# Kernel tuning notes

Hardware: AMD Instinct MI355X
Metric: run time of the kernel (lower is better)

Reference implementation:

```python
import jax, jax.numpy as jnp
import numpy as np

EMBED_DIM = 128
HIDDEN = 64
LN_EPS = 1e-5
NORM_EPS = 1e-6


def setup_inputs() -> dict:
    key = jax.random.key(0)
    ks = jax.random.split(key, 12)
    B, L = 32, 2048
    inp = {
        "map_lane_positions": jax.random.normal(ks[0], (B, L, 10, 2), dtype=jnp.float32),
        "map_is_intersection": jax.random.randint(ks[1], (B, L), 0, 3, dtype=jnp.int64),
        "map_turn_direction": jax.random.randint(ks[2], (B, L), 0, 3, dtype=jnp.int64),
        "map_traffic_control": jax.random.randint(ks[3], (B, L), 0, 2, dtype=jnp.int64),
        # SingleInputEmbedding params: Linear(2,64) -> LayerNorm(64) -> ReLU -> Linear(64,128)
        "W1": jax.random.normal(ks[4], (2, HIDDEN), dtype=jnp.float32) * 0.5,
        "b1": jax.random.normal(ks[5], (HIDDEN,), dtype=jnp.float32) * 0.1,
        "ln_gamma": jnp.ones((HIDDEN,), dtype=jnp.float32),
        "ln_beta": jnp.zeros((HIDDEN,), dtype=jnp.float32),
        "W2": jax.random.normal(ks[6], (HIDDEN, EMBED_DIM), dtype=jnp.float32) * 0.1,
        "b2": jax.random.normal(ks[7], (EMBED_DIM,), dtype=jnp.float32) * 0.1,
        # discrete embedding tables
        "E_intersection": jax.random.normal(ks[8], (3, EMBED_DIM), dtype=jnp.float32),
        "E_turn": jax.random.normal(ks[9], (3, EMBED_DIM), dtype=jnp.float32),
        "E_traffic": jax.random.normal(ks[10], (2, EMBED_DIM), dtype=jnp.float32),
    }
    return inp


def _mlp(x, W1, b1, g, beta, W2, b2):
    h = x @ W1 + b1                                  # [..., 64]
    mu = jnp.mean(h, axis=-1, keepdims=True)
    var = jnp.mean((h - mu) ** 2, axis=-1, keepdims=True)
    h = (h - mu) * jax.lax.rsqrt(var + LN_EPS) * g + beta
    h = jax.nn.relu(h)
    return h @ W2 + b2                               # [..., 128]


def reference(map_lane_positions, map_is_intersection, map_turn_direction,
              map_traffic_control, W1, b1, ln_gamma, ln_beta, W2, b2,
              E_intersection, E_turn, E_traffic):
    # direction vectors between consecutive points: [B, L, 9, 2]
    dv = map_lane_positions[:, :, 1:, :] - map_lane_positions[:, :, :-1, :]
    norms = jnp.sqrt(jnp.sum(dv ** 2, axis=-1, keepdims=True) + NORM_EPS)
    dv = dv / norms

    cont = _mlp(dv, W1, b1, ln_gamma, ln_beta, W2, b2)   # [B, L, 9, 128]
    # discrete embeddings broadcast over the 9-point axis
    disc = (E_intersection[map_is_intersection]
            + E_turn[map_turn_direction]
            + E_traffic[map_traffic_control])             # [B, L, 128]
    fused = cont + disc[:, :, None, :]                    # [B, L, 9, 128]
    return jnp.max(fused, axis=2)                         # [B, L, 128]
```

## Files before the change

kernel.cpp:

```cpp
#include <hip/hip_runtime.h>
#include <hip/hip_bf16.h>

#define NB      16
#define THREADS 256

#define WS_CST4   0
#define WS_QUAD   256
#define WS_DISC   272
#define WS_W2     2576

typedef float f32x4  __attribute__((ext_vector_type(4)));
typedef short bf16x8 __attribute__((ext_vector_type(8)));

static __device__ __forceinline__ unsigned f2bf(float f) {
    __hip_bfloat16 h = __float2bfloat16(f);
    return (unsigned)__builtin_bit_cast(unsigned short, h);
}

__global__ __launch_bounds__(THREADS)
void lane_setup_kernel(const float* __restrict__ W1, const float* __restrict__ b1,
                       const float* __restrict__ gam, const float* __restrict__ bet,
                       const float* __restrict__ W2, const float* __restrict__ b2,
                       const float* __restrict__ Ei, const float* __restrict__ Et,
                       const float* __restrict__ Etc, float* __restrict__ ws)
{
    const int tid = threadIdx.x, lane = tid & 63, wv = tid >> 6;

    if (wv == 0) {
        float wx = W1[lane], wy = W1[64 + lane], bb = b1[lane];
        float sx = wx, sy = wy, sb = bb;
        #pragma unroll
        for (int m = 1; m < 64; m <<= 1) {
            sx += __shfl_xor(sx, m, 64);
            sy += __shfl_xor(sy, m, 64);
            sb += __shfl_xor(sb, m, 64);
        }
        float a = wx - sx * (1.f / 64.f);
        float b = wy - sy * (1.f / 64.f);
        float c = bb - sb * (1.f / 64.f);
        float p0 = a * a, p1 = b * b, p2 = a * b, p3 = a * c, p4 = b * c, p5 = c * c;
        #pragma unroll
        for (int m = 1; m < 64; m <<= 1) {
            p0 += __shfl_xor(p0, m, 64); p1 += __shfl_xor(p1, m, 64);
            p2 += __shfl_xor(p2, m, 64); p3 += __shfl_xor(p3, m, 64);
            p4 += __shfl_xor(p4, m, 64); p5 += __shfl_xor(p5, m, 64);
        }
        float g = gam[lane];
        ((float4*)(ws + WS_CST4))[lane] = make_float4(a * g, b * g, c * g, bet[lane]);
        if (lane == 0) {
            ws[WS_QUAD + 0] = p0 * (1.f / 64.f);
            ws[WS_QUAD + 1] = p1 * (1.f / 64.f);
            ws[WS_QUAD + 2] = p2 * (1.f / 64.f);
            ws[WS_QUAD + 3] = p3 * (1.f / 64.f);
            ws[WS_QUAD + 4] = p4 * (1.f / 64.f);
            ws[WS_QUAD + 5] = p5 * (1.f / 64.f) + 1e-5f;
        }
    }

    {
        uint4* dst = (uint4*)(ws + WS_W2);
        #pragma unroll
        for (int f = wv * 4; f < wv * 4 + 4; ++f) {
            int c = f >> 1, kt = f & 1;
            int col = c * 16 + (lane & 15);
            int k0  = kt * 32 + (lane >> 4) * 8;
            unsigned w[4];
            #pragma unroll
            for (int j = 0; j < 4; ++j) {
                unsigned lo = f2bf(W2[(k0 + 2 * j) * 128 + col]);
                unsigned hi = f2bf(W2[(k0 + 2 * j + 1) * 128 + col]);
                w[j] = (hi << 16) | lo;
            }
            dst[f * 64 + lane] = make_uint4(w[0], w[1], w[2], w[3]);
        }
    }

    for (int i = tid; i < 18 * 128; i += THREADS) {
        int combo = i >> 7, col = i & 127;
        int ai = combo / 6; int r = combo - ai * 6; int bi = r >> 1; int ci = r & 1;
        ws[WS_DISC + i] = b2[col] + Ei[ai * 128 + col] + Et[bi * 128 + col] + Etc[ci * 128 + col];
    }
}

__global__ __launch_bounds__(THREADS)
void lane_node_embed_mfma(const float* __restrict__ pos,
                          const int*   __restrict__ idx_int,
                          const int*   __restrict__ idx_turn,
                          const int*   __restrict__ idx_tc,
                          const float* __restrict__ ws,
                          float* __restrict__ out,
                          int n_nodes)
{
    __shared__ __align__(16) unsigned short H[NB * 9 * 64];
    __shared__ float4 smv[NB * 9];
    __shared__ int    cmb_lds[NB];

    const int tid  = threadIdx.x;
    const int lane = tid & 63;
    const int wv   = __builtin_amdgcn_readfirstlane(tid >> 6);
    const int blockStart = blockIdx.x * NB;

    if (tid < NB * 9) {
        int nd = tid / 9, p = tid - nd * 9;
        int gn = blockStart + nd;
        float ax = 0.f, ay = 0.f, is = 0.f;
        if (gn < n_nodes) {
            const float2* pp = (const float2*)pos + (size_t)gn * 10 + p;
            float2 q0 = pp[0], q1 = pp[1];
            float dx = q1.x - q0.x, dy = q1.y - q0.y;
            float inv = rsqrtf(fmaf(dx, dx, fmaf(dy, dy, 1e-6f)));
            dx *= inv; dy *= inv;
            float qA = ws[WS_QUAD + 0], qB = ws[WS_QUAD + 1], qC = ws[WS_QUAD + 2];
            float qD = ws[WS_QUAD + 3], qE = ws[WS_QUAD + 4], qF = ws[WS_QUAD + 5];
            float t   = fmaf(dx * dy, qC, fmaf(dx, qD, dy * qE));
            float var = fmaf(2.f, t, fmaf(dx * dx, qA, fmaf(dy * dy, qB, qF)));
            is = rsqrtf(var);
            ax = dx * is; ay = dy * is;
        }
        smv[tid] = make_float4(ax, ay, is, 0.f);
    }
    if (tid < NB) {
        int gn = blockStart + tid;
        cmb_lds[tid] = (gn < n_nodes)
            ? (idx_int[gn] * 3 + idx_turn[gn]) * 2 + idx_tc[gn] : 0;
    }

    const int kl   = lane & 31;
    const int half = lane >> 5;
    const float4 cstA = ((const float4*)(ws + WS_CST4))[2 * kl];
    const float4 cstB = ((const float4*)(ws + WS_CST4))[2 * kl + 1];

    const int ct0 = wv * 2;
    const uint4* wfr = (const uint4*)(ws + WS_W2);
    bf16x8 Bfr[2][2];
    #pragma unroll
    for (int c = 0; c < 2; ++c)
        #pragma unroll
        for (int kt = 0; kt < 2; ++kt)
            Bfr[c][kt] = __builtin_bit_cast(bf16x8, wfr[((ct0 + c) * 2 + kt) * 64 + lane]);

    __syncthreads();

    {
        const int kch  = kl >> 2;
        const int kofs = (2 * kl) & 7;
        #pragma unroll
        for (int i = 0; i < 2; ++i) {
            int nd = wv * 4 + 2 * i + half;
            int basew = nd * 576 + ((kch ^ (nd & 7)) << 3) + kofs;
            #pragma unroll
            for (int p = 0; p < 9; ++p) {
                float4 t = smv[nd * 9 + p];
                float a = fmaf(t.x, cstA.x, fmaf(t.y, cstA.y, fmaf(t.z, cstA.z, cstA.w)));
                float b = fmaf(t.x, cstB.x, fmaf(t.y, cstB.y, fmaf(t.z, cstB.z, cstB.w)));
                a = fmaxf(a, 0.f); b = fmaxf(b, 0.f);
                *(unsigned*)&H[basew + p * 64] = (f2bf(b) << 16) | f2bf(a);
            }
        }
    }
    __syncthreads();

    const int g   = lane >> 4;
    const int l15 = lane & 15;
    const int sr  = l15 & 7;
    const int i0  = l15 * 576 + ((g ^ sr) << 3);
    const int i1  = l15 * 576 + (((4 + g) ^ sr) << 3);

    int cjv[4];
    #pragma unroll
    for (int jj = 0; jj < 4; ++jj) cjv[jj] = cmb_lds[g * 4 + jj];
    float dvp[2][4];
    #pragma unroll
    for (int c = 0; c < 2; ++c)
        #pragma unroll
        for (int jj = 0; jj < 4; ++jj)
            dvp[c][jj] = ws[WS_DISC + cjv[jj] * 128 + (ct0 + c) * 16 + l15];

    f32x4 mx0 = {-INFINITY, -INFINITY, -INFINITY, -INFINITY};
    f32x4 mx1 = mx0;
    const f32x4 zz = {0.f, 0.f, 0.f, 0.f};
    #pragma unroll
    for (int p = 0; p < 9; ++p) {
        bf16x8 a0 = *(const bf16x8*)&H[i0 + p * 64];
        bf16x8 a1 = *(const bf16x8*)&H[i1 + p * 64];
        f32x4 t0 = __builtin_amdgcn_mfma_f32_16x16x32_bf16(a0, Bfr[0][0], zz, 0, 0, 0);
        t0       = __builtin_amdgcn_mfma_f32_16x16x32_bf16(a1, Bfr[0][1], t0, 0, 0, 0);
        f32x4 t1 = __builtin_amdgcn_mfma_f32_16x16x32_bf16(a0, Bfr[1][0], zz, 0, 0, 0);
        t1       = __builtin_amdgcn_mfma_f32_16x16x32_bf16(a1, Bfr[1][1], t1, 0, 0, 0);
        #pragma unroll
        for (int k = 0; k < 4; ++k) {
            mx0[k] = fmaxf(mx0[k], t0[k]);
            mx1[k] = fmaxf(mx1[k], t1[k]);
        }
    }

    #pragma unroll
    for (int c = 0; c < 2; ++c) {
        int col = (ct0 + c) * 16 + l15;
        f32x4 m = (c == 0) ? mx0 : mx1;
        #pragma unroll
        for (int j = 0; j < 4; ++j) {
            int gn = blockStart + g * 4 + j;
            if (gn < n_nodes)
                out[(size_t)gn * 128 + col] = m[j] + dvp[c][j];
        }
    }
}

extern "C" void kernel_launch(void* const* d_in, const int* in_sizes, int n_in,
                              void* d_out, int out_size, void* d_ws, size_t ws_size,
                              hipStream_t stream) {
    const float* pos  = (const float*)d_in[0];
    const int*   ii   = (const int*)  d_in[1];
    const int*   it   = (const int*)  d_in[2];
    const int*   itc  = (const int*)  d_in[3];
    const float* W1   = (const float*)d_in[4];
    const float* b1   = (const float*)d_in[5];
    const float* gam  = (const float*)d_in[6];
    const float* bet  = (const float*)d_in[7];
    const float* W2   = (const float*)d_in[8];
    const float* b2   = (const float*)d_in[9];
    const float* Ei   = (const float*)d_in[10];
    const float* Et   = (const float*)d_in[11];
    const float* Etc  = (const float*)d_in[12];
    float* out = (float*)d_out;
    float* ws  = (float*)d_ws;

    int n_nodes = in_sizes[1];
    int blocks  = (n_nodes + NB - 1) / NB;

    hipLaunchKernelGGL(lane_setup_kernel, dim3(1), dim3(THREADS), 0, stream,
                       W1, b1, gam, bet, W2, b2, Ei, Et, Etc, ws);
    hipLaunchKernelGGL(lane_node_embed_mfma, dim3(blocks), dim3(THREADS), 0, stream,
                       pos, ii, it, itc, ws, out, n_nodes);
}
```

Baseline: 30.45 us.

## Swap MFMA operands for float4 stores, use wave shuffles instead of LDS staging

The main kernel swaps the A/B operands of the MFMA so each lane holds four consecutive output columns of one node. The output store becomes a single float4 write per column tile, and the discrete-embedding gather becomes one float4 load per tile. The LDS staging of per-point direction vectors and combo indices, plus one __syncthreads, is replaced by per-wave computation and __shfl broadcasts, with the LN inverse-std recomputed by sqrt from the scaled vector. The setup kernel is split across 6 blocks so its three parts run in parallel, at the cost of an extra sqrt per point and duplicated index loads.

```diff
diff --git a/kernel.cpp b/kernel.cpp
--- a/kernel.cpp
+++ b/kernel.cpp
@@ -25,8 +25,9 @@
                        const float* __restrict__ Etc, float* __restrict__ ws)
 {
     const int tid = threadIdx.x, lane = tid & 63, wv = tid >> 6;
-
-    if (wv == 0) {
+    const int b = blockIdx.x;
+
+    if (b == 0 && wv == 0) {
         float wx = W1[lane], wy = W1[64 + lane], bb = b1[lane];
         float sx = wx, sy = wy, sb = bb;
         #pragma unroll
@@ -36,9 +37,9 @@
             sb += __shfl_xor(sb, m, 64);
         }
         float a = wx - sx * (1.f / 64.f);
-        float b = wy - sy * (1.f / 64.f);
+        float bc = wy - sy * (1.f / 64.f);
         float c = bb - sb * (1.f / 64.f);
-        float p0 = a * a, p1 = b * b, p2 = a * b, p3 = a * c, p4 = b * c, p5 = c * c;
+        float p0 = a * a, p1 = bc * bc, p2 = a * bc, p3 = a * c, p4 = bc * c, p5 = c * c;
         #pragma unroll
         for (int m = 1; m < 64; m <<= 1) {
             p0 += __shfl_xor(p0, m, 64); p1 += __shfl_xor(p1, m, 64);
@@ -46,7 +47,7 @@
             p4 += __shfl_xor(p4, m, 64); p5 += __shfl_xor(p5, m, 64);
         }
         float g = gam[lane];
-        ((float4*)(ws + WS_CST4))[lane] = make_float4(a * g, b * g, c * g, bet[lane]);
+        ((float4*)(ws + WS_CST4))[lane] = make_float4(a * g, bc * g, c * g, bet[lane]);
         if (lane == 0) {
             ws[WS_QUAD + 0] = p0 * (1.f / 64.f);
             ws[WS_QUAD + 1] = p1 * (1.f / 64.f);
@@ -55,30 +56,26 @@
             ws[WS_QUAD + 4] = p4 * (1.f / 64.f);
             ws[WS_QUAD + 5] = p5 * (1.f / 64.f) + 1e-5f;
         }
-    }
-
-    {
+    } else if (b >= 1 && b <= 4) {
         uint4* dst = (uint4*)(ws + WS_W2);
-        #pragma unroll
-        for (int f = wv * 4; f < wv * 4 + 4; ++f) {
-            int c = f >> 1, kt = f & 1;
-            int col = c * 16 + (lane & 15);
-            int k0  = kt * 32 + (lane >> 4) * 8;
-            unsigned w[4];
-            #pragma unroll
-            for (int j = 0; j < 4; ++j) {
-                unsigned lo = f2bf(W2[(k0 + 2 * j) * 128 + col]);
-                unsigned hi = f2bf(W2[(k0 + 2 * j + 1) * 128 + col]);
-                w[j] = (hi << 16) | lo;
-            }
-            dst[f * 64 + lane] = make_uint4(w[0], w[1], w[2], w[3]);
-        }
-    }
-
-    for (int i = tid; i < 18 * 128; i += THREADS) {
-        int combo = i >> 7, col = i & 127;
-        int ai = combo / 6; int r = combo - ai * 6; int bi = r >> 1; int ci = r & 1;
-        ws[WS_DISC + i] = b2[col] + Ei[ai * 128 + col] + Et[bi * 128 + col] + Etc[ci * 128 + col];
+        int f = (b - 1) * 4 + wv;
+        int c = f >> 1, kt = f & 1;
+        int col = c * 16 + (lane & 15);
+        int k0  = kt * 32 + (lane >> 4) * 8;
+        unsigned w[4];
+        #pragma unroll
+        for (int j = 0; j < 4; ++j) {
+            unsigned lo = f2bf(W2[(k0 + 2 * j) * 128 + col]);
+            unsigned hi = f2bf(W2[(k0 + 2 * j + 1) * 128 + col]);
+            w[j] = (hi << 16) | lo;
+        }
+        dst[f * 64 + lane] = make_uint4(w[0], w[1], w[2], w[3]);
+    } else if (b == 5) {
+        for (int i = tid; i < 18 * 128; i += THREADS) {
+            int combo = i >> 7, col = i & 127;
+            int ai = combo / 6; int r = combo - ai * 6; int bi = r >> 1; int ci = r & 1;
+            ws[WS_DISC + i] = b2[col] + Ei[ai * 128 + col] + Et[bi * 128 + col] + Etc[ci * 128 + col];
+        }
     }
 }
 
@@ -92,20 +89,22 @@
                           int n_nodes)
 {
     __shared__ __align__(16) unsigned short H[NB * 9 * 64];
-    __shared__ float4 smv[NB * 9];
-    __shared__ int    cmb_lds[NB];
 
     const int tid  = threadIdx.x;
     const int lane = tid & 63;
     const int wv   = __builtin_amdgcn_readfirstlane(tid >> 6);
     const int blockStart = blockIdx.x * NB;
 
-    if (tid < NB * 9) {
-        int nd = tid / 9, p = tid - nd * 9;
-        int gn = blockStart + nd;
-        float ax = 0.f, ay = 0.f, is = 0.f;
-        if (gn < n_nodes) {
-            const float2* pp = (const float2*)pos + (size_t)gn * 10 + p;
+    const int l15 = lane & 15;
+    const int g   = lane >> 4;
+
+    const int sn = lane / 9;
+    const int sp = lane - sn * 9;
+    float ax_own = 0.f, ay_own = 0.f;
+    {
+        int gn = blockStart + wv * 4 + sn;
+        if (lane < 36 && gn < n_nodes) {
+            const float2* pp = (const float2*)pos + (size_t)gn * 10 + sp;
             float2 q0 = pp[0], q1 = pp[1];
             float dx = q1.x - q0.x, dy = q1.y - q0.y;
             float inv = rsqrtf(fmaf(dx, dx, fmaf(dy, dy, 1e-6f)));
@@ -114,16 +113,15 @@
             float qD = ws[WS_QUAD + 3], qE = ws[WS_QUAD + 4], qF = ws[WS_QUAD + 5];
             float t   = fmaf(dx * dy, qC, fmaf(dx, qD, dy * qE));
             float var = fmaf(2.f, t, fmaf(dx * dx, qA, fmaf(dy * dy, qB, qF)));
-            is = rsqrtf(var);
-            ax = dx * is; ay = dy * is;
-        }
-        smv[tid] = make_float4(ax, ay, is, 0.f);
-    }
-    if (tid < NB) {
-        int gn = blockStart + tid;
-        cmb_lds[tid] = (gn < n_nodes)
-            ? (idx_int[gn] * 3 + idx_turn[gn]) * 2 + idx_tc[gn] : 0;
-    }
+            float is0 = rsqrtf(var);
+            ax_own = dx * is0; ay_own = dy * is0;
+        }
+    }
+
+    const int gn15 = blockStart + l15;
+    int cmb = 0;
+    if (gn15 < n_nodes)
+        cmb = (idx_int[gn15] * 3 + idx_turn[gn15]) * 2 + idx_tc[gn15];
 
     const int kl   = lane & 31;
     const int half = lane >> 5;
@@ -132,27 +130,34 @@
 
     const int ct0 = wv * 2;
     const uint4* wfr = (const uint4*)(ws + WS_W2);
-    bf16x8 Bfr[2][2];
+    bf16x8 Wfr[2][2];
     #pragma unroll
     for (int c = 0; c < 2; ++c)
         #pragma unroll
         for (int kt = 0; kt < 2; ++kt)
-            Bfr[c][kt] = __builtin_bit_cast(bf16x8, wfr[((ct0 + c) * 2 + kt) * 64 + lane]);
-
-    __syncthreads();
+            Wfr[c][kt] = __builtin_bit_cast(bf16x8, wfr[((ct0 + c) * 2 + kt) * 64 + lane]);
+
+    float4 dvp[2];
+    #pragma unroll
+    for (int c = 0; c < 2; ++c)
+        dvp[c] = *(const float4*)&ws[WS_DISC + cmb * 128 + (ct0 + c) * 16 + 4 * g];
 
     {
         const int kch  = kl >> 2;
         const int kofs = (2 * kl) & 7;
         #pragma unroll
         for (int i = 0; i < 2; ++i) {
-            int nd = wv * 4 + 2 * i + half;
+            int ndl = 2 * i + half;
+            int nd  = wv * 4 + ndl;
             int basew = nd * 576 + ((kch ^ (nd & 7)) << 3) + kofs;
             #pragma unroll
             for (int p = 0; p < 9; ++p) {
-                float4 t = smv[nd * 9 + p];
-                float a = fmaf(t.x, cstA.x, fmaf(t.y, cstA.y, fmaf(t.z, cstA.z, cstA.w)));
-                float b = fmaf(t.x, cstB.x, fmaf(t.y, cstB.y, fmaf(t.z, cstB.z, cstB.w)));
+                int o = ndl * 9 + p;
+                float ax = __shfl(ax_own, o, 64);
+                float ay = __shfl(ay_own, o, 64);
+                float is = sqrtf(fmaf(ax, ax, ay * ay));
+                float a = fmaf(ax, cstA.x, fmaf(ay, cstA.y, fmaf(is, cstA.z, cstA.w)));
+                float b = fmaf(ax, cstB.x, fmaf(ay, cstB.y, fmaf(is, cstB.z, cstB.w)));
                 a = fmaxf(a, 0.f); b = fmaxf(b, 0.f);
                 *(unsigned*)&H[basew + p * 64] = (f2bf(b) << 16) | f2bf(a);
             }
@@ -160,33 +165,21 @@
     }
     __syncthreads();
 
-    const int g   = lane >> 4;
-    const int l15 = lane & 15;
     const int sr  = l15 & 7;
     const int i0  = l15 * 576 + ((g ^ sr) << 3);
     const int i1  = l15 * 576 + (((4 + g) ^ sr) << 3);
-
-    int cjv[4];
-    #pragma unroll
-    for (int jj = 0; jj < 4; ++jj) cjv[jj] = cmb_lds[g * 4 + jj];
-    float dvp[2][4];
-    #pragma unroll
-    for (int c = 0; c < 2; ++c)
-        #pragma unroll
-        for (int jj = 0; jj < 4; ++jj)
-            dvp[c][jj] = ws[WS_DISC + cjv[jj] * 128 + (ct0 + c) * 16 + l15];
 
     f32x4 mx0 = {-INFINITY, -INFINITY, -INFINITY, -INFINITY};
     f32x4 mx1 = mx0;
     const f32x4 zz = {0.f, 0.f, 0.f, 0.f};
     #pragma unroll
     for (int p = 0; p < 9; ++p) {
-        bf16x8 a0 = *(const bf16x8*)&H[i0 + p * 64];
-        bf16x8 a1 = *(const bf16x8*)&H[i1 + p * 64];
-        f32x4 t0 = __builtin_amdgcn_mfma_f32_16x16x32_bf16(a0, Bfr[0][0], zz, 0, 0, 0);
-        t0       = __builtin_amdgcn_mfma_f32_16x16x32_bf16(a1, Bfr[0][1], t0, 0, 0, 0);
-        f32x4 t1 = __builtin_amdgcn_mfma_f32_16x16x32_bf16(a0, Bfr[1][0], zz, 0, 0, 0);
-        t1       = __builtin_amdgcn_mfma_f32_16x16x32_bf16(a1, Bfr[1][1], t1, 0, 0, 0);
+        bf16x8 h0 = *(const bf16x8*)&H[i0 + p * 64];
+        bf16x8 h1 = *(const bf16x8*)&H[i1 + p * 64];
+        f32x4 t0 = __builtin_amdgcn_mfma_f32_16x16x32_bf16(Wfr[0][0], h0, zz, 0, 0, 0);
+        t0       = __builtin_amdgcn_mfma_f32_16x16x32_bf16(Wfr[0][1], h1, t0, 0, 0, 0);
+        f32x4 t1 = __builtin_amdgcn_mfma_f32_16x16x32_bf16(Wfr[1][0], h0, zz, 0, 0, 0);
+        t1       = __builtin_amdgcn_mfma_f32_16x16x32_bf16(Wfr[1][1], h1, t1, 0, 0, 0);
         #pragma unroll
         for (int k = 0; k < 4; ++k) {
             mx0[k] = fmaxf(mx0[k], t0[k]);
@@ -194,15 +187,13 @@
         }
     }
 
-    #pragma unroll
-    for (int c = 0; c < 2; ++c) {
-        int col = (ct0 + c) * 16 + l15;
-        f32x4 m = (c == 0) ? mx0 : mx1;
-        #pragma unroll
-        for (int j = 0; j < 4; ++j) {
-            int gn = blockStart + g * 4 + j;
-            if (gn < n_nodes)
-                out[(size_t)gn * 128 + col] = m[j] + dvp[c][j];
+    if (gn15 < n_nodes) {
+        #pragma unroll
+        for (int c = 0; c < 2; ++c) {
+            f32x4 m = (c == 0) ? mx0 : mx1;
+            float4 v = make_float4(m[0] + dvp[c].x, m[1] + dvp[c].y,
+                                   m[2] + dvp[c].z, m[3] + dvp[c].w);
+            *(float4*)&out[(size_t)gn15 * 128 + (ct0 + c) * 16 + 4 * g] = v;
         }
     }
 }
@@ -229,7 +220,7 @@
     int n_nodes = in_sizes[1];
     int blocks  = (n_nodes + NB - 1) / NB;
 
-    hipLaunchKernelGGL(lane_setup_kernel, dim3(1), dim3(THREADS), 0, stream,
+    hipLaunchKernelGGL(lane_setup_kernel, dim3(6), dim3(THREADS), 0, stream,
                        W1, b1, gam, bet, W2, b2, Ei, Et, Etc, ws);
     hipLaunchKernelGGL(lane_node_embed_mfma, dim3(blocks), dim3(THREADS), 0, stream,
                        pos, ii, it, itc, ws, out, n_nodes);
```

New measurement: 38.88 us. +27.7%, slower.

## Compute direction vectors per lane in registers and split setup across blocks

Applied to the files above, without the earlier changes.

The main kernel no longer runs a separate phase that computes normalized direction vectors and LayerNorm scale into shared memory behind a barrier. Each lane now loads its node's ten points as float4 vectors and recomputes the direction, normalization and inverse std itself, which removes one __syncthreads and the smv LDS traffic at the cost of redundant math across the 32 lanes sharing a node. The setup kernel is also spread over six blocks so the W2 packing and discrete-table summation run in parallel rather than serially in one block.

```diff
diff --git a/kernel.cpp b/kernel.cpp
--- a/kernel.cpp
+++ b/kernel.cpp
@@ -25,8 +25,9 @@
                        const float* __restrict__ Etc, float* __restrict__ ws)
 {
     const int tid = threadIdx.x, lane = tid & 63, wv = tid >> 6;
-
-    if (wv == 0) {
+    const int b = blockIdx.x;
+
+    if (b == 0 && wv == 0) {
         float wx = W1[lane], wy = W1[64 + lane], bb = b1[lane];
         float sx = wx, sy = wy, sb = bb;
         #pragma unroll
@@ -36,9 +37,9 @@
             sb += __shfl_xor(sb, m, 64);
         }
         float a = wx - sx * (1.f / 64.f);
-        float b = wy - sy * (1.f / 64.f);
+        float bc = wy - sy * (1.f / 64.f);
         float c = bb - sb * (1.f / 64.f);
-        float p0 = a * a, p1 = b * b, p2 = a * b, p3 = a * c, p4 = b * c, p5 = c * c;
+        float p0 = a * a, p1 = bc * bc, p2 = a * bc, p3 = a * c, p4 = bc * c, p5 = c * c;
         #pragma unroll
         for (int m = 1; m < 64; m <<= 1) {
             p0 += __shfl_xor(p0, m, 64); p1 += __shfl_xor(p1, m, 64);
@@ -46,7 +47,7 @@
             p4 += __shfl_xor(p4, m, 64); p5 += __shfl_xor(p5, m, 64);
         }
         float g = gam[lane];
-        ((float4*)(ws + WS_CST4))[lane] = make_float4(a * g, b * g, c * g, bet[lane]);
+        ((float4*)(ws + WS_CST4))[lane] = make_float4(a * g, bc * g, c * g, bet[lane]);
         if (lane == 0) {
             ws[WS_QUAD + 0] = p0 * (1.f / 64.f);
             ws[WS_QUAD + 1] = p1 * (1.f / 64.f);
@@ -55,30 +56,26 @@
             ws[WS_QUAD + 4] = p4 * (1.f / 64.f);
             ws[WS_QUAD + 5] = p5 * (1.f / 64.f) + 1e-5f;
         }
-    }
-
-    {
+    } else if (b >= 1 && b <= 4) {
         uint4* dst = (uint4*)(ws + WS_W2);
-        #pragma unroll
-        for (int f = wv * 4; f < wv * 4 + 4; ++f) {
-            int c = f >> 1, kt = f & 1;
-            int col = c * 16 + (lane & 15);
-            int k0  = kt * 32 + (lane >> 4) * 8;
-            unsigned w[4];
-            #pragma unroll
-            for (int j = 0; j < 4; ++j) {
-                unsigned lo = f2bf(W2[(k0 + 2 * j) * 128 + col]);
-                unsigned hi = f2bf(W2[(k0 + 2 * j + 1) * 128 + col]);
-                w[j] = (hi << 16) | lo;
-            }
-            dst[f * 64 + lane] = make_uint4(w[0], w[1], w[2], w[3]);
-        }
-    }
-
-    for (int i = tid; i < 18 * 128; i += THREADS) {
-        int combo = i >> 7, col = i & 127;
-        int ai = combo / 6; int r = combo - ai * 6; int bi = r >> 1; int ci = r & 1;
-        ws[WS_DISC + i] = b2[col] + Ei[ai * 128 + col] + Et[bi * 128 + col] + Etc[ci * 128 + col];
+        int f = (b - 1) * 4 + wv;
+        int c = f >> 1, kt = f & 1;
+        int col = c * 16 + (lane & 15);
+        int k0  = kt * 32 + (lane >> 4) * 8;
+        unsigned w[4];
+        #pragma unroll
+        for (int j = 0; j < 4; ++j) {
+            unsigned lo = f2bf(W2[(k0 + 2 * j) * 128 + col]);
+            unsigned hi = f2bf(W2[(k0 + 2 * j + 1) * 128 + col]);
+            w[j] = (hi << 16) | lo;
+        }
+        dst[f * 64 + lane] = make_uint4(w[0], w[1], w[2], w[3]);
+    } else if (b == 5) {
+        for (int i = tid; i < 18 * 128; i += THREADS) {
+            int combo = i >> 7, col = i & 127;
+            int ai = combo / 6; int r = combo - ai * 6; int bi = r >> 1; int ci = r & 1;
+            ws[WS_DISC + i] = b2[col] + Ei[ai * 128 + col] + Et[bi * 128 + col] + Etc[ci * 128 + col];
+        }
     }
 }
 
@@ -92,39 +89,22 @@
                           int n_nodes)
 {
     __shared__ __align__(16) unsigned short H[NB * 9 * 64];
-    __shared__ float4 smv[NB * 9];
-    __shared__ int    cmb_lds[NB];
+    __shared__ int cmb_lds[NB];
 
     const int tid  = threadIdx.x;
     const int lane = tid & 63;
     const int wv   = __builtin_amdgcn_readfirstlane(tid >> 6);
     const int blockStart = blockIdx.x * NB;
 
-    if (tid < NB * 9) {
-        int nd = tid / 9, p = tid - nd * 9;
-        int gn = blockStart + nd;
-        float ax = 0.f, ay = 0.f, is = 0.f;
-        if (gn < n_nodes) {
-            const float2* pp = (const float2*)pos + (size_t)gn * 10 + p;
-            float2 q0 = pp[0], q1 = pp[1];
-            float dx = q1.x - q0.x, dy = q1.y - q0.y;
-            float inv = rsqrtf(fmaf(dx, dx, fmaf(dy, dy, 1e-6f)));
-            dx *= inv; dy *= inv;
-            float qA = ws[WS_QUAD + 0], qB = ws[WS_QUAD + 1], qC = ws[WS_QUAD + 2];
-            float qD = ws[WS_QUAD + 3], qE = ws[WS_QUAD + 4], qF = ws[WS_QUAD + 5];
-            float t   = fmaf(dx * dy, qC, fmaf(dx, qD, dy * qE));
-            float var = fmaf(2.f, t, fmaf(dx * dx, qA, fmaf(dy * dy, qB, qF)));
-            is = rsqrtf(var);
-            ax = dx * is; ay = dy * is;
-        }
-        smv[tid] = make_float4(ax, ay, is, 0.f);
-    }
     if (tid < NB) {
         int gn = blockStart + tid;
         cmb_lds[tid] = (gn < n_nodes)
             ? (idx_int[gn] * 3 + idx_turn[gn]) * 2 + idx_tc[gn] : 0;
     }
 
+    const float qA = ws[WS_QUAD + 0], qB = ws[WS_QUAD + 1], qC = ws[WS_QUAD + 2];
+    const float qD = ws[WS_QUAD + 3], qE = ws[WS_QUAD + 4], qF = ws[WS_QUAD + 5];
+
     const int kl   = lane & 31;
     const int half = lane >> 5;
     const float4 cstA = ((const float4*)(ws + WS_CST4))[2 * kl];
@@ -139,20 +119,42 @@
         for (int kt = 0; kt < 2; ++kt)
             Bfr[c][kt] = __builtin_bit_cast(bf16x8, wfr[((ct0 + c) * 2 + kt) * 64 + lane]);
 
-    __syncthreads();
-
     {
         const int kch  = kl >> 2;
         const int kofs = (2 * kl) & 7;
         #pragma unroll
         for (int i = 0; i < 2; ++i) {
             int nd = wv * 4 + 2 * i + half;
+            int gn = blockStart + nd;
             int basew = nd * 576 + ((kch ^ (nd & 7)) << 3) + kofs;
+
+            float4 P[5];
+            if (gn < n_nodes) {
+                const float4* pb = (const float4*)(pos + (size_t)gn * 20);
+                #pragma unroll
+                for (int j = 0; j < 5; ++j) P[j] = pb[j];
+            } else {
+                #pragma unroll
+                for (int j = 0; j < 5; ++j) P[j] = make_float4(0.f, 0.f, 0.f, 0.f);
+            }
+
             #pragma unroll
             for (int p = 0; p < 9; ++p) {
-                float4 t = smv[nd * 9 + p];
-                float a = fmaf(t.x, cstA.x, fmaf(t.y, cstA.y, fmaf(t.z, cstA.z, cstA.w)));
-                float b = fmaf(t.x, cstB.x, fmaf(t.y, cstB.y, fmaf(t.z, cstB.z, cstB.w)));
+                float x0, y0, x1, y1;
+                if ((p & 1) == 0) { x0 = P[p >> 1].x; y0 = P[p >> 1].y;
+                                    x1 = P[p >> 1].z; y1 = P[p >> 1].w; }
+                else              { x0 = P[p >> 1].z; y0 = P[p >> 1].w;
+                                    x1 = P[(p + 1) >> 1].x; y1 = P[(p + 1) >> 1].y; }
+                float dx = x1 - x0, dy = y1 - y0;
+                float inv = rsqrtf(fmaf(dx, dx, fmaf(dy, dy, 1e-6f)));
+                dx *= inv; dy *= inv;
+                float tt  = fmaf(dx * dy, qC, fmaf(dx, qD, dy * qE));
+                float var = fmaf(2.f, tt, fmaf(dx * dx, qA, fmaf(dy * dy, qB, qF)));
+                float is  = rsqrtf(var);
+                float ax = dx * is, ay = dy * is;
+
+                float a = fmaf(ax, cstA.x, fmaf(ay, cstA.y, fmaf(is, cstA.z, cstA.w)));
+                float b = fmaf(ax, cstB.x, fmaf(ay, cstB.y, fmaf(is, cstB.z, cstB.w)));
                 a = fmaxf(a, 0.f); b = fmaxf(b, 0.f);
                 *(unsigned*)&H[basew + p * 64] = (f2bf(b) << 16) | f2bf(a);
             }
@@ -229,7 +231,7 @@
     int n_nodes = in_sizes[1];
     int blocks  = (n_nodes + NB - 1) / NB;
 
-    hipLaunchKernelGGL(lane_setup_kernel, dim3(1), dim3(THREADS), 0, stream,
+    hipLaunchKernelGGL(lane_setup_kernel, dim3(6), dim3(THREADS), 0, stream,
                        W1, b1, gam, bet, W2, b2, Ei, Et, Etc, ws);
     hipLaunchKernelGGL(lane_node_embed_mfma, dim3(blocks), dim3(THREADS), 0, stream,
                        pos, ii, it, itc, ws, out, n_nodes);
```

New measurement: 39.83 us. +30.8%, slower.

## Halve nodes per block and split setup kernel across six blocks

Applied to the files above, without the earlier changes.

The main kernel now processes 8 nodes per 128-thread block instead of 16 per 256. Each wave computes four column tiles in two passes, and half of each MFMA's 16 rows are duplicates whose results are discarded. The setup kernel is split across 6 blocks so the LayerNorm constants, the W2 bf16 fragment packing and the discrete-embedding table are built in parallel rather than serially by one block. This trades wasted MFMA work for twice as many blocks, which should give better occupancy and load balance across CUs, plus a shorter setup kernel.

```diff
diff --git a/kernel.cpp b/kernel.cpp
--- a/kernel.cpp
+++ b/kernel.cpp
@@ -1,8 +1,8 @@
 #include <hip/hip_runtime.h>
 #include <hip/hip_bf16.h>
 
-#define NB      16
-#define THREADS 256
+#define NB      8
+#define THREADS 128
 
 #define WS_CST4   0
 #define WS_QUAD   256
@@ -17,7 +17,7 @@
     return (unsigned)__builtin_bit_cast(unsigned short, h);
 }
 
-__global__ __launch_bounds__(THREADS)
+__global__ __launch_bounds__(256)
 void lane_setup_kernel(const float* __restrict__ W1, const float* __restrict__ b1,
                        const float* __restrict__ gam, const float* __restrict__ bet,
                        const float* __restrict__ W2, const float* __restrict__ b2,
@@ -25,8 +25,9 @@
                        const float* __restrict__ Etc, float* __restrict__ ws)
 {
     const int tid = threadIdx.x, lane = tid & 63, wv = tid >> 6;
-
-    if (wv == 0) {
+    const int b = blockIdx.x;
+
+    if (b == 0 && wv == 0) {
         float wx = W1[lane], wy = W1[64 + lane], bb = b1[lane];
         float sx = wx, sy = wy, sb = bb;
         #pragma unroll
@@ -36,9 +37,9 @@
             sb += __shfl_xor(sb, m, 64);
         }
         float a = wx - sx * (1.f / 64.f);
-        float b = wy - sy * (1.f / 64.f);
+        float bc = wy - sy * (1.f / 64.f);
         float c = bb - sb * (1.f / 64.f);
-        float p0 = a * a, p1 = b * b, p2 = a * b, p3 = a * c, p4 = b * c, p5 = c * c;
+        float p0 = a * a, p1 = bc * bc, p2 = a * bc, p3 = a * c, p4 = bc * c, p5 = c * c;
         #pragma unroll
         for (int m = 1; m < 64; m <<= 1) {
             p0 += __shfl_xor(p0, m, 64); p1 += __shfl_xor(p1, m, 64);
@@ -46,7 +47,7 @@
             p4 += __shfl_xor(p4, m, 64); p5 += __shfl_xor(p5, m, 64);
         }
         float g = gam[lane];
-        ((float4*)(ws + WS_CST4))[lane] = make_float4(a * g, b * g, c * g, bet[lane]);
+        ((float4*)(ws + WS_CST4))[lane] = make_float4(a * g, bc * g, c * g, bet[lane]);
         if (lane == 0) {
             ws[WS_QUAD + 0] = p0 * (1.f / 64.f);
             ws[WS_QUAD + 1] = p1 * (1.f / 64.f);
@@ -55,30 +56,26 @@
             ws[WS_QUAD + 4] = p4 * (1.f / 64.f);
             ws[WS_QUAD + 5] = p5 * (1.f / 64.f) + 1e-5f;
         }
-    }
-
-    {
+    } else if (b >= 1 && b <= 4) {
         uint4* dst = (uint4*)(ws + WS_W2);
-        #pragma unroll
-        for (int f = wv * 4; f < wv * 4 + 4; ++f) {
-            int c = f >> 1, kt = f & 1;
-            int col = c * 16 + (lane & 15);
-            int k0  = kt * 32 + (lane >> 4) * 8;
-            unsigned w[4];
-            #pragma unroll
-            for (int j = 0; j < 4; ++j) {
-                unsigned lo = f2bf(W2[(k0 + 2 * j) * 128 + col]);
-                unsigned hi = f2bf(W2[(k0 + 2 * j + 1) * 128 + col]);
-                w[j] = (hi << 16) | lo;
-            }
-            dst[f * 64 + lane] = make_uint4(w[0], w[1], w[2], w[3]);
-        }
-    }
-
-    for (int i = tid; i < 18 * 128; i += THREADS) {
-        int combo = i >> 7, col = i & 127;
-        int ai = combo / 6; int r = combo - ai * 6; int bi = r >> 1; int ci = r & 1;
-        ws[WS_DISC + i] = b2[col] + Ei[ai * 128 + col] + Et[bi * 128 + col] + Etc[ci * 128 + col];
+        int f = (b - 1) * 4 + wv;
+        int c = f >> 1, kt = f & 1;
+        int col = c * 16 + (lane & 15);
+        int k0  = kt * 32 + (lane >> 4) * 8;
+        unsigned w[4];
+        #pragma unroll
+        for (int j = 0; j < 4; ++j) {
+            unsigned lo = f2bf(W2[(k0 + 2 * j) * 128 + col]);
+            unsigned hi = f2bf(W2[(k0 + 2 * j + 1) * 128 + col]);
+            w[j] = (hi << 16) | lo;
+        }
+        dst[f * 64 + lane] = make_uint4(w[0], w[1], w[2], w[3]);
+    } else if (b == 5) {
+        for (int i = tid; i < 18 * 128; i += 256) {
+            int combo = i >> 7, col = i & 127;
+            int ai = combo / 6; int r = combo - ai * 6; int bi = r >> 1; int ci = r & 1;
+            ws[WS_DISC + i] = b2[col] + Ei[ai * 128 + col] + Et[bi * 128 + col] + Etc[ci * 128 + col];
+        }
     }
 }
 
@@ -130,24 +127,16 @@
     const float4 cstA = ((const float4*)(ws + WS_CST4))[2 * kl];
     const float4 cstB = ((const float4*)(ws + WS_CST4))[2 * kl + 1];
 
-    const int ct0 = wv * 2;
-    const uint4* wfr = (const uint4*)(ws + WS_W2);
-    bf16x8 Bfr[2][2];
-    #pragma unroll
-    for (int c = 0; c < 2; ++c)
-        #pragma unroll
-        for (int kt = 0; kt < 2; ++kt)
-            Bfr[c][kt] = __builtin_bit_cast(bf16x8, wfr[((ct0 + c) * 2 + kt) * 64 + lane]);
-
     __syncthreads();
 
     {
+        const int h2   = wv * 2 + half;
         const int kch  = kl >> 2;
         const int kofs = (2 * kl) & 7;
         #pragma unroll
         for (int i = 0; i < 2; ++i) {
-            int nd = wv * 4 + 2 * i + half;
-            int basew = nd * 576 + ((kch ^ (nd & 7)) << 3) + kofs;
+            int nd = i * 4 + h2;
+            int basew = nd * 576 + ((kch ^ nd) << 3) + kofs;
             #pragma unroll
             for (int p = 0; p < 9; ++p) {
                 float4 t = smv[nd * 9 + p];
@@ -162,47 +151,66 @@
 
     const int g   = lane >> 4;
     const int l15 = lane & 15;
-    const int sr  = l15 & 7;
-    const int i0  = l15 * 576 + ((g ^ sr) << 3);
-    const int i1  = l15 * 576 + (((4 + g) ^ sr) << 3);
+    const int nd8 = l15 & 7;
+    const int i0  = nd8 * 576 + ((g ^ nd8) << 3);
+    const int i1  = nd8 * 576 + (((4 + g) ^ nd8) << 3);
+    const int ct0 = wv * 4;
+
+    const uint4* wfr = (const uint4*)(ws + WS_W2);
+    const f32x4 zz = {0.f, 0.f, 0.f, 0.f};
+    const bool rowsValid = (g < 2);
 
     int cjv[4];
     #pragma unroll
-    for (int jj = 0; jj < 4; ++jj) cjv[jj] = cmb_lds[g * 4 + jj];
-    float dvp[2][4];
+    for (int jj = 0; jj < 4; ++jj) cjv[jj] = cmb_lds[(g * 4 + jj) & 7];
+
     #pragma unroll
-    for (int c = 0; c < 2; ++c)
-        #pragma unroll
-        for (int jj = 0; jj < 4; ++jj)
-            dvp[c][jj] = ws[WS_DISC + cjv[jj] * 128 + (ct0 + c) * 16 + l15];
-
-    f32x4 mx0 = {-INFINITY, -INFINITY, -INFINITY, -INFINITY};
-    f32x4 mx1 = mx0;
-    const f32x4 zz = {0.f, 0.f, 0.f, 0.f};
-    #pragma unroll
-    for (int p = 0; p < 9; ++p) {
-        bf16x8 a0 = *(const bf16x8*)&H[i0 + p * 64];
-        bf16x8 a1 = *(const bf16x8*)&H[i1 + p * 64];
-        f32x4 t0 = __builtin_amdgcn_mfma_f32_16x16x32_bf16(a0, Bfr[0][0], zz, 0, 0, 0);
-        t0       = __builtin_amdgcn_mfma_f32_16x16x32_bf16(a1, Bfr[0][1], t0, 0, 0, 0);
-        f32x4 t1 = __builtin_amdgcn_mfma_f32_16x16x32_bf16(a0, Bfr[1][0], zz, 0, 0, 0);
-        t1       = __builtin_amdgcn_mfma_f32_16x16x32_bf16(a1, Bfr[1][1], t1, 0, 0, 0);
-        #pragma unroll
-        for (int k = 0; k < 4; ++k) {
-            mx0[k] = fmaxf(mx0[k], t0[k]);
-            mx1[k] = fmaxf(mx1[k], t1[k]);
-        }
-    }
-
-    #pragma unroll
-    for (int c = 0; c < 2; ++c) {
-        int col = (ct0 + c) * 16 + l15;
-        f32x4 m = (c == 0) ? mx0 : mx1;
-        #pragma unroll
-        for (int j = 0; j < 4; ++j) {
-            int gn = blockStart + g * 4 + j;
-            if (gn < n_nodes)
-                out[(size_t)gn * 128 + col] = m[j] + dvp[c][j];
+    for (int cg = 0; cg < 2; ++cg) {
+        bf16x8 B[2][2];
+        #pragma unroll
+        for (int c = 0; c < 2; ++c)
+            #pragma unroll
+            for (int kt = 0; kt < 2; ++kt)
+                B[c][kt] = __builtin_bit_cast(bf16x8,
+                               wfr[((ct0 + cg * 2 + c) * 2 + kt) * 64 + lane]);
+
+        float dvp[2][4];
+        #pragma unroll
+        for (int c = 0; c < 2; ++c)
+            #pragma unroll
+            for (int jj = 0; jj < 4; ++jj)
+                dvp[c][jj] = rowsValid
+                    ? ws[WS_DISC + cjv[jj] * 128 + (ct0 + cg * 2 + c) * 16 + l15] : 0.f;
+
+        f32x4 mx0 = {-INFINITY, -INFINITY, -INFINITY, -INFINITY};
+        f32x4 mx1 = mx0;
+        #pragma unroll
+        for (int p = 0; p < 9; ++p) {
+            bf16x8 a0 = *(const bf16x8*)&H[i0 + p * 64];
+            bf16x8 a1 = *(const bf16x8*)&H[i1 + p * 64];
+            f32x4 t0 = __builtin_amdgcn_mfma_f32_16x16x32_bf16(a0, B[0][0], zz, 0, 0, 0);
+            t0       = __builtin_amdgcn_mfma_f32_16x16x32_bf16(a1, B[0][1], t0, 0, 0, 0);
+            f32x4 t1 = __builtin_amdgcn_mfma_f32_16x16x32_bf16(a0, B[1][0], zz, 0, 0, 0);
+            t1       = __builtin_amdgcn_mfma_f32_16x16x32_bf16(a1, B[1][1], t1, 0, 0, 0);
+            #pragma unroll
+            for (int k = 0; k < 4; ++k) {
+                mx0[k] = fmaxf(mx0[k], t0[k]);
+                mx1[k] = fmaxf(mx1[k], t1[k]);
+            }
+        }
+
+        if (rowsValid) {
+            #pragma unroll
+            for (int c = 0; c < 2; ++c) {
+                int col = (ct0 + cg * 2 + c) * 16 + l15;
+                f32x4 m = (c == 0) ? mx0 : mx1;
+                #pragma unroll
+                for (int j = 0; j < 4; ++j) {
+                    int gn = blockStart + g * 4 + j;
+                    if (gn < n_nodes)
+                        out[(size_t)gn * 128 + col] = m[j] + dvp[c][j];
+                }
+            }
         }
     }
 }
@@ -229,7 +237,7 @@
     int n_nodes = in_sizes[1];
     int blocks  = (n_nodes + NB - 1) / NB;
 
-    hipLaunchKernelGGL(lane_setup_kernel, dim3(1), dim3(THREADS), 0, stream,
+    hipLaunchKernelGGL(lane_setup_kernel, dim3(6), dim3(256), 0, stream,
                        W1, b1, gam, bet, W2, b2, Ei, Et, Etc, ws);
     hipLaunchKernelGGL(lane_node_embed_mfma, dim3(blocks), dim3(THREADS), 0, stream,
                        pos, ii, it, itc, ws, out, n_nodes);
```

New measurement: 41.25 us. 35.5% more time.
